# Kernel tuning notes

Hardware: AMD Instinct MI355X
Metric: run time of the kernel (lower is better)

## Reference

```python
import jax, jax.numpy as jnp
import numpy as np

ALPHA = 0.8  # STE clipping threshold (unused in fwd-only path)


def binary_sign(x):
    # torch: x.sign() with zeros mapped to +1 => where(x >= 0, 1, -1)
    return jnp.where(x >= 0, jnp.ones((), x.dtype), -jnp.ones((), x.dtype))


def setup_inputs() -> dict:
    key = jax.random.key(0)
    ks = jax.random.split(key, 5)
    B, D = 16384, 4096
    x = jax.random.normal(ks[0], (B, D), dtype=jnp.float32)
    w0 = jax.random.normal(ks[1], (D, D), dtype=jnp.float32) * 0.1
    w1 = jax.random.normal(ks[2], (D, D), dtype=jnp.float32) * 0.1
    w2 = jax.random.normal(ks[3], (D, D), dtype=jnp.float32) * 0.1
    w3 = jax.random.normal(ks[4], (1, D), dtype=jnp.float32) * 0.1
    b0 = jnp.zeros((D,), jnp.float32)
    b1 = jnp.zeros((D,), jnp.float32)
    b2 = jnp.zeros((D,), jnp.float32)
    b3 = jnp.zeros((1,), jnp.float32)
    return {"x": x, "w0": w0, "b0": b0, "w1": w1, "b1": b1,
            "w2": w2, "b2": b2, "w3": w3, "b3": b3}


def reference(x, w0, b0, w1, b1, w2, b2, w3, b3):
    h = x
    for w, b in ((w0, b0), (w1, b1), (w2, b2), (w3, b3)):
        # BinaryLinear: binarize weights, dense matmul, add bias
        z = jnp.einsum('bi,oi->bo', h, binary_sign(w)) + b
        # BinaryActivation: binarize pre-activation
        h = binary_sign(z)
    return h  # [B, 1]
```

## Files before the change

kernel.cpp:

```cpp
#include <hip/hip_runtime.h>

typedef int   v4i  __attribute__((ext_vector_type(4)));
typedef int   v16i __attribute__((ext_vector_type(16)));
typedef float f4   __attribute__((ext_vector_type(4)));

#define DD 4096
#define BATCH 16384
#define FIXCAP (1u << 22)

__device__ __forceinline__ void gload16(const void* g, void* l) {
  __builtin_amdgcn_global_load_lds((const __attribute__((address_space(1))) void*)g,
                                   (__attribute__((address_space(3))) void*)l, 16, 0, 0);
}
#define ASM_VMCNT(n) asm volatile("s_waitcnt vmcnt(" #n ")" ::: "memory")
#define ASM_LGKM0()  asm volatile("s_waitcnt lgkmcnt(0)" ::: "memory")
#define BARF()       asm volatile("s_barrier" ::: "memory")

__device__ __forceinline__ int swz2(int row) { return ((row >> 1) & 3) ^ ((row >> 3) & 1); }

__global__ void binarize_swz_k(const float* __restrict__ w, unsigned char* __restrict__ o,
                               int swz_on) {
  int T = blockIdx.x * blockDim.x + threadIdx.x;
  int row = T >> 10, rem = T & 1023;
  int kblk = rem >> 4, seg = (rem >> 2) & 3, q = rem & 3;
  f4 v = *(const f4*)(w + (size_t)row * DD + kblk * 64 + seg * 16 + q * 4);
  unsigned int r = 0;
#pragma unroll
  for (int j = 0; j < 4; ++j) {
    unsigned int b = (v[j] >= 0.0f) ? 0x01u : 0xFFu;
    r |= b << (8 * j);
  }
  int slot = swz_on ? (seg ^ swz2(row)) : seg;
  *(unsigned int*)(o + (size_t)row * DD + kblk * 64 + slot * 16 + q * 4) = r;
}

__global__ void rowsum_k(const unsigned char* __restrict__ wb, int* __restrict__ R) {
  int lane = threadIdx.x & 63, wid = threadIdx.x >> 6;
  int row = blockIdx.x * 4 + wid;
  const unsigned char* p = wb + (size_t)row * DD;
  int s = 0;
#pragma unroll
  for (int j = 0; j < 4; ++j) {
    v4i a = *(const v4i*)(p + lane * 16 + j * 1024);
#pragma unroll
    for (int w = 0; w < 4; ++w) {
      unsigned int xa = (unsigned int)a[w];
#pragma unroll
      for (int by = 0; by < 4; ++by)
        s += (int)(signed char)((xa >> (8 * by)) & 255u);
    }
  }
#pragma unroll
  for (int off = 32; off > 0; off >>= 1) s += __shfl_down(s, off);
  if (lane == 0) R[row] = s;
}

__global__ void digitize3_k(const float* __restrict__ x, unsigned char* __restrict__ Xp) {
  int T = blockIdx.x * blockDim.x + threadIdx.x;
  int row = T >> 10, rem = T & 1023;
  int kblk = rem >> 4, seg = (rem >> 2) & 3, q = rem & 3;
  f4 v = *(const f4*)(x + (size_t)row * DD + kblk * 64 + seg * 16 + q * 4);
  unsigned int Y[4];
#pragma unroll
  for (int j = 0; j < 4; ++j) {
    int X = (int)(v[j] * 524288.0f);
    Y[j] = (unsigned int)(X + 8388608);
  }
  int slot = seg ^ swz2(row);
  size_t base = (size_t)row * DD + kblk * 64 + slot * 16 + q * 4;
#pragma unroll
  for (int d = 0; d < 3; ++d) {
    unsigned int wv = ((Y[0] >> (8 * d)) & 255u)
                    | (((Y[1] >> (8 * d)) & 255u) << 8)
                    | (((Y[2] >> (8 * d)) & 255u) << 16)
                    | (((Y[3] >> (8 * d)) & 255u) << 24);
    wv ^= 0x80808080u;
    *(unsigned int*)(Xp + (size_t)d * (64u << 20) + base) = wv;
  }
}

__global__ void zeroc_k(unsigned int* c) { if (threadIdx.x == 0) *c = 0; }

__global__ __launch_bounds__(256, 2) void gemm0p3_k(
    const unsigned char* __restrict__ Xp, const unsigned char* __restrict__ wb,
    const int* __restrict__ R, const float* __restrict__ bias,
    signed char* __restrict__ h1,
    unsigned int* __restrict__ wl, unsigned int* __restrict__ cnt) {
  __shared__ __align__(16) unsigned char Asp[2][3][64 * 64];
  __shared__ __align__(16) unsigned char Bs[2][128 * 64];
  const int tid = threadIdx.x, lane = tid & 63, wid = tid >> 6;
  const int wm = wid >> 1, wn = wid & 1;
  const int bid = blockIdx.x;
  const int xcd = bid & 7, sl = bid >> 3;
  const int m0 = ((xcd << 5) + (sl >> 5)) << 6;
  const int n0 = (sl & 31) << 7;

  v16i acc[3][2];
#pragma unroll
  for (int d = 0; d < 3; ++d)
#pragma unroll
    for (int f = 0; f < 2; ++f)
#pragma unroll
      for (int e = 0; e < 16; ++e) acc[d][f][e] = 0;

  auto stage = [&](int bf, int kb) {
#pragma unroll
    for (int i = 0; i < 3; ++i) {
      int c = wid * 3 + i;
      int d = c >> 2, sub = c & 3;
      int lrow = sub * 16 + (lane >> 2);
      const unsigned char* g = Xp + (size_t)d * (64u << 20)
                             + (size_t)(m0 + lrow) * 4096 + kb * 64 + (lane & 3) * 16;
      gload16(g, &Asp[bf][d][sub * 1024]);
    }
#pragma unroll
    for (int j = 0; j < 2; ++j) {
      int c = wid * 2 + j;
      int lrowB = c * 16 + (lane >> 2);
      const unsigned char* gB = wb + (size_t)(n0 + lrowB) * 4096 + kb * 64 + (lane & 3) * 16;
      gload16(gB, &Bs[bf][c * 1024]);
    }
  };

  const int rl = lane & 31, hi = lane >> 5;
  const int arow = wm * 32 + rl;
  const int asw = swz2(arow);
  const int brow0 = wn * 64 + rl, brow1 = wn * 64 + 32 + rl;
  const int bsw0 = swz2(brow0), bsw1 = swz2(brow1);

  stage(0, 0);
  stage(1, 1);
  ASM_VMCNT(5); BARF();
  int cur = 0;
  for (int t = 0; t < 64; ++t) {
    v4i af[2][3], bg[2][2];
#pragma unroll
    for (int kt = 0; kt < 2; ++kt) {
      int g = kt * 2 + hi;
#pragma unroll
      for (int d = 0; d < 3; ++d)
        af[kt][d] = *(const v4i*)&Asp[cur][d][arow * 64 + ((g ^ asw) * 16)];
      bg[kt][0] = *(const v4i*)&Bs[cur][brow0 * 64 + ((g ^ bsw0) * 16)];
      bg[kt][1] = *(const v4i*)&Bs[cur][brow1 * 64 + ((g ^ bsw1) * 16)];
    }
    ASM_LGKM0(); BARF();
    if (t < 62) stage(cur, t + 2);
    __builtin_amdgcn_s_setprio(1);
#pragma unroll
    for (int kt = 0; kt < 2; ++kt)
#pragma unroll
      for (int d = 0; d < 3; ++d)
#pragma unroll
        for (int f = 0; f < 2; ++f)
          acc[d][f] = __builtin_amdgcn_mfma_i32_32x32x32_i8(af[kt][d], bg[kt][f], acc[d][f], 0, 0, 0);
    __builtin_amdgcn_s_setprio(0);
    if (t < 62) { ASM_VMCNT(5); BARF(); }
    else if (t == 62) { ASM_VMCNT(0); BARF(); }
    cur ^= 1;
  }

#pragma unroll
  for (int f = 0; f < 2; ++f) {
    int col = n0 + wn * 64 + f * 32 + (lane & 31);
    long long rterm = 32896LL * (long long)R[col];
    double bb = (double)bias[col];
#pragma unroll
    for (int r = 0; r < 16; ++r) {
      long long Z = (long long)acc[0][f][r] + 256LL * (long long)acc[1][f][r]
                  + 65536LL * (long long)acc[2][f][r] + rterm;
      double z = (double)Z * 1.9073486328125e-6 + bb;
      int row = m0 + wm * 32 + (r & 3) + 8 * (r >> 2) + 4 * (lane >> 5);
      int col2 = col ^ (swz2(row) << 4);
      h1[(size_t)row * DD + col2] = (z >= 0.0) ? (signed char)1 : (signed char)(-1);
      if (fabs(z) <= 0.0079) {
        unsigned int idx = atomicAdd(cnt, 1u);
        if (idx < FIXCAP) wl[idx] = ((unsigned int)row << 12) | (unsigned int)col;
      }
    }
  }
}

__global__ void fixup_k(const float* __restrict__ x, const unsigned char* __restrict__ wb,
                        const float* __restrict__ bias, const unsigned int* __restrict__ wl,
                        const unsigned int* __restrict__ cnt, signed char* __restrict__ h1) {
  unsigned int n = *cnt; if (n > FIXCAP) n = FIXCAP;
  int lane = threadIdx.x & 63;
  int gw = (blockIdx.x * blockDim.x + threadIdx.x) >> 6;
  int nw = (gridDim.x * blockDim.x) >> 6;
  for (unsigned int e = gw; e < n; e += nw) {
    unsigned int ent = wl[e];
    int row = ent >> 12, col = ent & 4095;
    const float* xr = x + (size_t)row * DD;
    const unsigned char* wr = wb + (size_t)col * DD;
    int sw = swz2(col);
    long long s = 0;
#pragma unroll 4
    for (int j = 0; j < 64; ++j) {
      int k = j * 64 + lane;
      int kk = (k & ~63) + ((((k >> 4) & 3) ^ sw) * 16) + (k & 15);
      signed char w = (signed char)wr[kk];
      long long X = (long long)(int)(xr[k] * 134217728.0f);
      s += (w > 0) ? X : -X;
    }
#pragma unroll
    for (int off = 32; off > 0; off >>= 1) s += __shfl_down(s, off);
    if (lane == 0) {
      double z = (double)s * 7.450580596923828125e-9 + (double)bias[col];
      int col2 = col ^ (swz2(row) << 4);
      h1[(size_t)row * DD + col2] = (z >= 0.0) ? (signed char)1 : (signed char)(-1);
    }
  }
}

__global__ __launch_bounds__(512, 2) void gemm0f_k(
    const float* __restrict__ x, const unsigned char* __restrict__ wb,
    const int* __restrict__ R, const float* __restrict__ bias,
    signed char* __restrict__ h1) {
  __shared__ signed char As[2][4][128 * 80];
  __shared__ signed char Bs[2][128 * 80];
  const int tid = threadIdx.x;
  const int lane = tid & 63, wid = tid >> 6;
  const int wm = wid >> 1, wn = wid & 1;
  const int n0 = blockIdx.x * 128, m0 = blockIdx.y * 128;

  v16i acc[4][2];
#pragma unroll
  for (int d = 0; d < 4; ++d)
#pragma unroll
    for (int f = 0; f < 2; ++f)
#pragma unroll
      for (int e = 0; e < 16; ++e) acc[d][f][e] = 0;

  const int arow_l = tid >> 4, aseg = tid & 15;
  const int brow = tid >> 2,  bseg = (tid & 3) * 16;
  f4 va[4]; v4i vb;

  auto loadTile = [&](int kpos) {
#pragma unroll
    for (int p = 0; p < 4; ++p)
      va[p] = *(const f4*)(x + (size_t)(m0 + p * 32 + arow_l) * DD + kpos + aseg * 4);
    vb = *(const v4i*)(wb + (size_t)(n0 + brow) * DD + kpos + bseg);
  };
  auto writeTile = [&](int bf) {
#pragma unroll
    for (int p = 0; p < 4; ++p) {
      int row = p * 32 + arow_l;
      unsigned int Y[4];
#pragma unroll
      for (int j = 0; j < 4; ++j) {
        int X = (int)(va[p][j] * 134217728.0f);
        Y[j] = (unsigned int)(X + 1073741824);
      }
#pragma unroll
      for (int k = 0; k < 4; ++k) {
        unsigned int wv = ((Y[0] >> (8 * k)) & 255u) | (((Y[1] >> (8 * k)) & 255u) << 8)
                        | (((Y[2] >> (8 * k)) & 255u) << 16) | (((Y[3] >> (8 * k)) & 255u) << 24);
        wv ^= 0x80808080u;
        *(unsigned int*)&As[bf][k][row * 80 + aseg * 4] = wv;
      }
    }
    *(v4i*)&Bs[bf][brow * 80 + bseg] = vb;
  };

  loadTile(0); writeTile(0);
  __syncthreads();
  for (int t = 0; t < 64; ++t) {
    int cur = t & 1;
    if (t < 63) loadTile((t + 1) * 64);
#pragma unroll
    for (int kt = 0; kt < 2; ++kt) {
      int g = kt * 2 + (lane >> 5);
      int ar = (wm * 32 + (lane & 31)) * 80 + g * 16;
      v4i a[4], b[2];
#pragma unroll
      for (int d = 0; d < 4; ++d) a[d] = *(const v4i*)&As[cur][d][ar];
#pragma unroll
      for (int f = 0; f < 2; ++f) {
        int br = wn * 64 + f * 32 + (lane & 31);
        int slotb = g ^ swz2(br);
        b[f] = *(const v4i*)&Bs[cur][br * 80 + slotb * 16];
      }
#pragma unroll
      for (int d = 0; d < 4; ++d)
#pragma unroll
        for (int f = 0; f < 2; ++f)
          acc[d][f] = __builtin_amdgcn_mfma_i32_32x32x32_i8(a[d], b[f], acc[d][f], 0, 0, 0);
    }
    if (t < 63) writeTile(cur ^ 1);
    __syncthreads();
  }

#pragma unroll
  for (int f = 0; f < 2; ++f) {
    int col = n0 + wn * 64 + f * 32 + (lane & 31);
    long long rterm = 1082163328LL * (long long)R[col];
    double bb = (double)bias[col];
#pragma unroll
    for (int r = 0; r < 16; ++r) {
      long long Z = (long long)acc[0][f][r] + 256LL * (long long)acc[1][f][r]
                  + 65536LL * (long long)acc[2][f][r] + 16777216LL * (long long)acc[3][f][r]
                  + rterm;
      double z = (double)Z * 7.450580596923828125e-9 + bb;
      int row = m0 + wm * 32 + (r & 3) + 8 * (r >> 2) + 4 * (lane >> 5);
      int col2 = col ^ (swz2(row) << 4);
      h1[(size_t)row * DD + col2] = (z >= 0.0) ? (signed char)1 : (signed char)(-1);
    }
  }
}

__global__ __launch_bounds__(128, 2) void gemm_bin_k(
    const unsigned char* __restrict__ A, const unsigned char* __restrict__ Bw,
    const float* __restrict__ bias, signed char* __restrict__ out) {
  __shared__ __align__(16) unsigned char As[2][128 * 64];
  __shared__ __align__(16) unsigned char Bs[2][128 * 64];
  const int tid = threadIdx.x, lane = tid & 63, wid = tid >> 6;
  const int bid = blockIdx.x;
  const int xcd = bid & 7, sl = bid >> 3;
  const int m0 = ((xcd << 4) + (sl >> 5)) << 7;
  const int n0 = (sl & 31) << 7;

  v16i acc[4][2];
#pragma unroll
  for (int mi = 0; mi < 4; ++mi)
#pragma unroll
    for (int f = 0; f < 2; ++f)
#pragma unroll
      for (int e = 0; e < 16; ++e) acc[mi][f][e] = 0;

  auto stage = [&](int bf, int kb) {
#pragma unroll
    for (int j = 0; j < 4; ++j) {
      int c = wid * 4 + j;
      int lrow = c * 16 + (lane >> 2);
      const unsigned char* gA = A + (size_t)(m0 + lrow) * 4096 + kb * 64 + (lane & 3) * 16;
      gload16(gA, &As[bf][c * 1024]);
    }
#pragma unroll
    for (int j = 0; j < 4; ++j) {
      int c = wid * 4 + j;
      int lrow = c * 16 + (lane >> 2);
      const unsigned char* gB = Bw + (size_t)(n0 + lrow) * 4096 + kb * 64 + (lane & 3) * 16;
      gload16(gB, &Bs[bf][c * 1024]);
    }
  };

  const int rl = lane & 31, hi = lane >> 5;
  const int brow0 = wid * 64 + rl, brow1 = wid * 64 + 32 + rl;
  const int bsw0 = swz2(brow0), bsw1 = swz2(brow1);

  stage(0, 0);
  stage(1, 1);
  ASM_VMCNT(8); BARF();
  int cur = 0;
  for (int t = 0; t < 64; ++t) {
    v4i af[2][4], bg[2][2];
#pragma unroll
    for (int kt = 0; kt < 2; ++kt) {
      int g = kt * 2 + hi;
#pragma unroll
      for (int mi = 0; mi < 4; ++mi) {
        int arow = mi * 32 + rl;
        af[kt][mi] = *(const v4i*)&As[cur][arow * 64 + ((g ^ swz2(arow)) * 16)];
      }
      bg[kt][0] = *(const v4i*)&Bs[cur][brow0 * 64 + ((g ^ bsw0) * 16)];
      bg[kt][1] = *(const v4i*)&Bs[cur][brow1 * 64 + ((g ^ bsw1) * 16)];
    }
    ASM_LGKM0(); BARF();
    if (t < 62) stage(cur, t + 2);
    __builtin_amdgcn_s_setprio(1);
#pragma unroll
    for (int kt = 0; kt < 2; ++kt)
#pragma unroll
      for (int mi = 0; mi < 4; ++mi)
#pragma unroll
        for (int f = 0; f < 2; ++f)
          acc[mi][f] = __builtin_amdgcn_mfma_i32_32x32x32_i8(af[kt][mi], bg[kt][f], acc[mi][f], 0, 0, 0);
    __builtin_amdgcn_s_setprio(0);
    if (t < 62) { ASM_VMCNT(8); BARF(); }
    else if (t == 62) { ASM_VMCNT(0); BARF(); }
    cur ^= 1;
  }

#pragma unroll
  for (int mi = 0; mi < 4; ++mi)
#pragma unroll
    for (int f = 0; f < 2; ++f) {
      int col = n0 + wid * 64 + f * 32 + (lane & 31);
      float bb = bias[col];
#pragma unroll
      for (int r = 0; r < 16; ++r) {
        float z = (float)acc[mi][f][r] + bb;
        int row = m0 + mi * 32 + (r & 3) + 8 * (r >> 2) + 4 * (lane >> 5);
        int col2 = col ^ (swz2(row) << 4);
        out[(size_t)row * DD + col2] = (z >= 0.0f) ? (signed char)1 : (signed char)(-1);
      }
    }
}

__global__ void final_k(const unsigned char* __restrict__ h, const unsigned char* __restrict__ w3b,
                        const float* __restrict__ b3, float* __restrict__ out) {
  int lane = threadIdx.x & 63, wid = threadIdx.x >> 6;
  int row = blockIdx.x * 4 + wid;
  int swz = swz2(row) << 4;
  const unsigned char* p = h + (size_t)row * DD;
  int s = 0;
#pragma unroll
  for (int j = 0; j < 4; ++j) {
    int e = lane * 16 + j * 1024;
    v4i a = *(const v4i*)(p + (e ^ swz));
    v4i b = *(const v4i*)(w3b + e);
#pragma unroll
    for (int w = 0; w < 4; ++w) {
      unsigned int xa = (unsigned int)a[w], xb = (unsigned int)b[w];
#pragma unroll
      for (int by = 0; by < 4; ++by)
        s += (int)(signed char)((xa >> (8 * by)) & 255u)
           * (int)(signed char)((xb >> (8 * by)) & 255u);
    }
  }
#pragma unroll
  for (int off = 32; off > 0; off >>= 1) s += __shfl_down(s, off);
  if (lane == 0) {
    float z = (float)s + b3[0];
    out[row] = (z >= 0.0f) ? 1.0f : -1.0f;
  }
}

extern "C" void kernel_launch(void* const* d_in, const int* in_sizes, int n_in,
                              void* d_out, int out_size, void* d_ws, size_t ws_size,
                              hipStream_t stream) {
  (void)in_sizes; (void)n_in; (void)out_size;
  const float* x  = (const float*)d_in[0];
  const float* w0 = (const float*)d_in[1];
  const float* b0 = (const float*)d_in[2];
  const float* w1 = (const float*)d_in[3];
  const float* b1 = (const float*)d_in[4];
  const float* w2 = (const float*)d_in[5];
  const float* b2 = (const float*)d_in[6];
  const float* w3 = (const float*)d_in[7];
  const float* b3 = (const float*)d_in[8];

  char* ws = (char*)d_ws;
  unsigned char* w0b = (unsigned char*)(ws + 0);
  unsigned char* w1b = (unsigned char*)(ws + (16ull << 20));
  unsigned char* w2b = (unsigned char*)(ws + (32ull << 20));
  unsigned char* w3b = (unsigned char*)(ws + (48ull << 20));
  int*           R   = (int*)(ws + (48ull << 20) + 65536);
  unsigned char* h1  = (unsigned char*)(ws + (64ull << 20));
  unsigned char* h2  = (unsigned char*)(ws + (128ull << 20));
  unsigned char* Xp  = (unsigned char*)(ws + (128ull << 20));
  unsigned int*  cnt = (unsigned int*)(ws + (320ull << 20));
  unsigned int*  wl  = (unsigned int*)(ws + (320ull << 20) + 64);
  float* out = (float*)d_out;

  binarize_swz_k<<<16384, 256, 0, stream>>>(w0, w0b, 1);
  binarize_swz_k<<<16384, 256, 0, stream>>>(w1, w1b, 1);
  binarize_swz_k<<<16384, 256, 0, stream>>>(w2, w2b, 1);
  binarize_swz_k<<<4,     256, 0, stream>>>(w3, w3b, 0);
  rowsum_k<<<1024, 256, 0, stream>>>(w0b, R);

  if (ws_size >= (384ull << 20)) {
    digitize3_k<<<65536, 256, 0, stream>>>(x, Xp);
    zeroc_k<<<1, 64, 0, stream>>>(cnt);
    gemm0p3_k<<<8192, 256, 0, stream>>>(Xp, w0b, R, b0, (signed char*)h1, wl, cnt);
    fixup_k<<<2048, 256, 0, stream>>>(x, w0b, b0, wl, cnt, (signed char*)h1);
  } else {
    gemm0f_k<<<dim3(32, 128), 512, 0, stream>>>(x, w0b, R, b0, (signed char*)h1);
  }
  gemm_bin_k<<<4096, 128, 0, stream>>>(h1, w1b, b1, (signed char*)h2);
  gemm_bin_k<<<4096, 128, 0, stream>>>(h2, w2b, b2, (signed char*)h1);
  final_k<<<4096, 256, 0, stream>>>(h1, w3b, b3, out);
}
```

Baseline: 1.785 ms.

## Triple-buffer LDS and split k-tile into two half-steps in binary GEMMs

Both int8 MFMA GEMM kernels move from double to triple LDS buffering. The next stage's global-to-LDS loads now target the buffer that was consumed two iterations earlier, so they can be issued right after the first barrier without waiting for the current tile's LDS reads. Each k-tile is split into two halves, with the second half's LDS reads interleaved after the first half's MFMAs, so register-fragment loads overlap with compute. The explicit lgkmcnt(0) wait is removed, and the kernels now use more shared memory, which may lower occupancy at two blocks per CU.

```diff
diff --git a/kernel.cpp b/kernel.cpp
--- a/kernel.cpp
+++ b/kernel.cpp
@@ -13,7 +13,6 @@
                                    (__attribute__((address_space(3))) void*)l, 16, 0, 0);
 }
 #define ASM_VMCNT(n) asm volatile("s_waitcnt vmcnt(" #n ")" ::: "memory")
-#define ASM_LGKM0()  asm volatile("s_waitcnt lgkmcnt(0)" ::: "memory")
 #define BARF()       asm volatile("s_barrier" ::: "memory")
 
 __device__ __forceinline__ int swz2(int row) { return ((row >> 1) & 3) ^ ((row >> 3) & 1); }
@@ -86,8 +85,8 @@
     const int* __restrict__ R, const float* __restrict__ bias,
     signed char* __restrict__ h1,
     unsigned int* __restrict__ wl, unsigned int* __restrict__ cnt) {
-  __shared__ __align__(16) unsigned char Asp[2][3][64 * 64];
-  __shared__ __align__(16) unsigned char Bs[2][128 * 64];
+  __shared__ __align__(16) unsigned char Asp[3][3][64 * 64];
+  __shared__ __align__(16) unsigned char Bs[3][128 * 64];
   const int tid = threadIdx.x, lane = tid & 63, wid = tid >> 6;
   const int wm = wid >> 1, wn = wid & 1;
   const int bid = blockIdx.x;
@@ -130,33 +129,48 @@
 
   stage(0, 0);
   stage(1, 1);
-  ASM_VMCNT(5); BARF();
-  int cur = 0;
+  ASM_VMCNT(0); BARF();
+  int p = 0;
   for (int t = 0; t < 64; ++t) {
-    v4i af[2][3], bg[2][2];
-#pragma unroll
-    for (int kt = 0; kt < 2; ++kt) {
-      int g = kt * 2 + hi;
+    const int s = (p >= 1) ? p - 1 : 2;
+    v4i af0[3], bg0[2];
+    {
+      int g = hi;
 #pragma unroll
       for (int d = 0; d < 3; ++d)
-        af[kt][d] = *(const v4i*)&Asp[cur][d][arow * 64 + ((g ^ asw) * 16)];
-      bg[kt][0] = *(const v4i*)&Bs[cur][brow0 * 64 + ((g ^ bsw0) * 16)];
-      bg[kt][1] = *(const v4i*)&Bs[cur][brow1 * 64 + ((g ^ bsw1) * 16)];
-    }
-    ASM_LGKM0(); BARF();
-    if (t < 62) stage(cur, t + 2);
+        af0[d] = *(const v4i*)&Asp[p][d][arow * 64 + ((g ^ asw) * 16)];
+      bg0[0] = *(const v4i*)&Bs[p][brow0 * 64 + ((g ^ bsw0) * 16)];
+      bg0[1] = *(const v4i*)&Bs[p][brow1 * 64 + ((g ^ bsw1) * 16)];
+    }
+    BARF();
+    if (t < 62) stage(s, t + 2);
     __builtin_amdgcn_s_setprio(1);
 #pragma unroll
-    for (int kt = 0; kt < 2; ++kt)
+    for (int d = 0; d < 3; ++d)
+#pragma unroll
+      for (int f = 0; f < 2; ++f)
+        acc[d][f] = __builtin_amdgcn_mfma_i32_32x32x32_i8(af0[d], bg0[f], acc[d][f], 0, 0, 0);
+    __builtin_amdgcn_s_setprio(0);
+    v4i af1[3], bg1[2];
+    {
+      int g = 2 + hi;
 #pragma unroll
       for (int d = 0; d < 3; ++d)
-#pragma unroll
-        for (int f = 0; f < 2; ++f)
-          acc[d][f] = __builtin_amdgcn_mfma_i32_32x32x32_i8(af[kt][d], bg[kt][f], acc[d][f], 0, 0, 0);
+        af1[d] = *(const v4i*)&Asp[p][d][arow * 64 + ((g ^ asw) * 16)];
+      bg1[0] = *(const v4i*)&Bs[p][brow0 * 64 + ((g ^ bsw0) * 16)];
+      bg1[1] = *(const v4i*)&Bs[p][brow1 * 64 + ((g ^ bsw1) * 16)];
+    }
+    if (t < 62) { ASM_VMCNT(5); }
+    else if (t == 62) { ASM_VMCNT(0); }
+    BARF();
+    __builtin_amdgcn_s_setprio(1);
+#pragma unroll
+    for (int d = 0; d < 3; ++d)
+#pragma unroll
+      for (int f = 0; f < 2; ++f)
+        acc[d][f] = __builtin_amdgcn_mfma_i32_32x32x32_i8(af1[d], bg1[f], acc[d][f], 0, 0, 0);
     __builtin_amdgcn_s_setprio(0);
-    if (t < 62) { ASM_VMCNT(5); BARF(); }
-    else if (t == 62) { ASM_VMCNT(0); BARF(); }
-    cur ^= 1;
+    p = (p < 2) ? p + 1 : 0;
   }
 
 #pragma unroll
@@ -311,8 +325,8 @@
 __global__ __launch_bounds__(128, 2) void gemm_bin_k(
     const unsigned char* __restrict__ A, const unsigned char* __restrict__ Bw,
     const float* __restrict__ bias, signed char* __restrict__ out) {
-  __shared__ __align__(16) unsigned char As[2][128 * 64];
-  __shared__ __align__(16) unsigned char Bs[2][128 * 64];
+  __shared__ __align__(16) unsigned char As[3][128 * 64];
+  __shared__ __align__(16) unsigned char Bs[3][128 * 64];
   const int tid = threadIdx.x, lane = tid & 63, wid = tid >> 6;
   const int bid = blockIdx.x;
   const int xcd = bid & 7, sl = bid >> 3;
@@ -350,35 +364,52 @@
 
   stage(0, 0);
   stage(1, 1);
-  ASM_VMCNT(8); BARF();
-  int cur = 0;
+  ASM_VMCNT(0); BARF();
+  int p = 0;
   for (int t = 0; t < 64; ++t) {
-    v4i af[2][4], bg[2][2];
-#pragma unroll
-    for (int kt = 0; kt < 2; ++kt) {
-      int g = kt * 2 + hi;
+    const int s = (p >= 1) ? p - 1 : 2;
+    v4i af0[4], bg0[2];
+    {
+      int g = hi;
 #pragma unroll
       for (int mi = 0; mi < 4; ++mi) {
         int arow = mi * 32 + rl;
-        af[kt][mi] = *(const v4i*)&As[cur][arow * 64 + ((g ^ swz2(arow)) * 16)];
-      }
-      bg[kt][0] = *(const v4i*)&Bs[cur][brow0 * 64 + ((g ^ bsw0) * 16)];
-      bg[kt][1] = *(const v4i*)&Bs[cur][brow1 * 64 + ((g ^ bsw1) * 16)];
-    }
-    ASM_LGKM0(); BARF();
-    if (t < 62) stage(cur, t + 2);
+        af0[mi] = *(const v4i*)&As[p][arow * 64 + ((g ^ swz2(arow)) * 16)];
+      }
+      bg0[0] = *(const v4i*)&Bs[p][brow0 * 64 + ((g ^ bsw0) * 16)];
+      bg0[1] = *(const v4i*)&Bs[p][brow1 * 64 + ((g ^ bsw1) * 16)];
+    }
+    BARF();
+    if (t < 62) stage(s, t + 2);
     __builtin_amdgcn_s_setprio(1);
 #pragma unroll
-    for (int kt = 0; kt < 2; ++kt)
-#pragma unroll
-      for (int mi = 0; mi < 4; ++mi)
-#pragma unroll
-        for (int f = 0; f < 2; ++f)
-          acc[mi][f] = __builtin_amdgcn_mfma_i32_32x32x32_i8(af[kt][mi], bg[kt][f], acc[mi][f], 0, 0, 0);
+    for (int mi = 0; mi < 4; ++mi)
+#pragma unroll
+      for (int f = 0; f < 2; ++f)
+        acc[mi][f] = __builtin_amdgcn_mfma_i32_32x32x32_i8(af0[mi], bg0[f], acc[mi][f], 0, 0, 0);
     __builtin_amdgcn_s_setprio(0);
-    if (t < 62) { ASM_VMCNT(8); BARF(); }
-    else if (t == 62) { ASM_VMCNT(0); BARF(); }
-    cur ^= 1;
+    v4i af1[4], bg1[2];
+    {
+      int g = 2 + hi;
+#pragma unroll
+      for (int mi = 0; mi < 4; ++mi) {
+        int arow = mi * 32 + rl;
+        af1[mi] = *(const v4i*)&As[p][arow * 64 + ((g ^ swz2(arow)) * 16)];
+      }
+      bg1[0] = *(const v4i*)&Bs[p][brow0 * 64 + ((g ^ bsw0) * 16)];
+      bg1[1] = *(const v4i*)&Bs[p][brow1 * 64 + ((g ^ bsw1) * 16)];
+    }
+    if (t < 62) { ASM_VMCNT(8); }
+    else if (t == 62) { ASM_VMCNT(0); }
+    BARF();
+    __builtin_amdgcn_s_setprio(1);
+#pragma unroll
+    for (int mi = 0; mi < 4; ++mi)
+#pragma unroll
+      for (int f = 0; f < 2; ++f)
+        acc[mi][f] = __builtin_amdgcn_mfma_i32_32x32x32_i8(af1[mi], bg1[f], acc[mi][f], 0, 0, 0);
+    __builtin_amdgcn_s_setprio(0);
+    p = (p < 2) ? p + 1 : 0;
   }
 
 #pragma unroll
```

New measurement: 1.925 ms. +7.8%, slower.
